# Kernel optimization log

Hardware: AMD Instinct MI355X
Metric: run time of the kernel (lower is better)

Reference implementation:

```python
import jax, jax.numpy as jnp
import numpy as np

N_BINS = 10


def setup_inputs() -> dict:
    key = jax.random.key(0)
    k1, k2 = jax.random.split(key)
    N, C = 1000000, 128
    logits = jax.random.normal(k1, (N, C), dtype=jnp.float32)
    labels = jax.random.randint(k2, (N,), 0, C, dtype=jnp.int64)
    return {"logits": logits, "labels": labels}


def reference(logits, labels):
    N = logits.shape[0]
    probs = jax.nn.softmax(logits, axis=1)
    confidences = jnp.max(probs, axis=1)          # [N]
    predictions = jnp.argmax(probs, axis=1)       # [N]
    accuracies = (predictions == labels).astype(jnp.float32)

    # Bin i covers (i/n, (i+1)/n]; ceil(conf*n)-1 gives that index.
    bin_idx = jnp.clip(
        jnp.ceil(confidences * N_BINS).astype(jnp.int32) - 1, 0, N_BINS - 1
    )

    counts = jax.ops.segment_sum(jnp.ones_like(confidences), bin_idx, num_segments=N_BINS)
    conf_sum = jax.ops.segment_sum(confidences, bin_idx, num_segments=N_BINS)
    acc_sum = jax.ops.segment_sum(accuracies, bin_idx, num_segments=N_BINS)

    prop_in_bin = counts / N
    nonempty = counts > 0
    denom = jnp.maximum(counts, 1.0)
    acc_in_bin = jnp.where(nonempty, acc_sum / denom, 0.0)
    conf_in_bin = jnp.where(nonempty, conf_sum / denom, 0.0)

    CE = conf_in_bin - acc_in_bin
    abs_CE = jnp.where(nonempty, jnp.abs(CE), 0.0)
    ece = jnp.sum(abs_CE * prop_in_bin)
    oe = jnp.sum(jnp.where(nonempty, conf_in_bin * jnp.maximum(CE, 0.0), 0.0) * prop_in_bin)

    # (ece, per-bin accuracy, oe, per-bin proportion, per-bin |CE|)
    return ece, acc_in_bin, oe, prop_in_bin, abs_CE
```

## Files before the change

### kernel.cpp

```cpp
#include <hip/hip_runtime.h>

#define N_BINS 10

template<int CTRL, bool BC>
__device__ __forceinline__ float dpp_f(float x, float old_) {
    int r = __builtin_amdgcn_update_dpp(__builtin_bit_cast(int, old_),
                                        __builtin_bit_cast(int, x),
                                        CTRL, 0xf, 0xf, BC);
    return __builtin_bit_cast(float, r);
}

__device__ __forceinline__ float half_reduce_add(float x) {
    x += dpp_f<0x111, true>(x, 0.f);
    x += dpp_f<0x112, true>(x, 0.f);
    x += dpp_f<0x114, true>(x, 0.f);
    x += dpp_f<0x118, true>(x, 0.f);
    x += dpp_f<0x142, true>(x, 0.f);
    return x;
}

__device__ __forceinline__ float half_reduce_max(float x) {
    x = fmaxf(x, dpp_f<0x111, false>(x, x));
    x = fmaxf(x, dpp_f<0x112, false>(x, x));
    x = fmaxf(x, dpp_f<0x114, false>(x, x));
    x = fmaxf(x, dpp_f<0x118, false>(x, x));
    x = fmaxf(x, dpp_f<0x142, false>(x, x));
    return x;
}

__global__ void ece_zero_ws(unsigned int* ws) {
    int i = threadIdx.x;
    if (i < 64) ws[i] = 0u;
}

__global__ __launch_bounds__(256) void ece_main(
        const float* __restrict__ logits,
        const int*   __restrict__ labels,
        float*       __restrict__ ws,
        int N) {
    __shared__ float              s_conf[N_BINS];
    __shared__ unsigned long long s_pack[N_BINS];
    if (threadIdx.x < N_BINS) {
        s_conf[threadIdx.x] = 0.f;
        s_pack[threadIdx.x] = 0ull;
    }
    __syncthreads();

    const int lane32       = threadIdx.x & 31;
    const int rowInBlock   = threadIdx.x >> 5;
    const int rowsPerBlock = blockDim.x >> 5;

    long long row = (long long)blockIdx.x * rowsPerBlock + rowInBlock;
    const long long rowStride = (long long)gridDim.x * rowsPerBlock;

    for (; row < N; row += rowStride) {
        const float4* p = (const float4*)(logits + row * 128);
        float4 v = p[lane32];
        int la = labels[row];

        float m4 = fmaxf(fmaxf(v.x, v.y), fmaxf(v.z, v.w));
        float e4 = __expf(v.x) + __expf(v.y) + __expf(v.z) + __expf(v.w);
        float vl = 0.f;
        if ((la >> 2) == lane32) {
            int r = la & 3;
            vl = (r == 0) ? v.x : (r == 1) ? v.y : (r == 2) ? v.z : v.w;
        }

        float S  = half_reduce_add(e4);
        float M  = half_reduce_max(m4);
        float VL = half_reduce_add(vl);

        if (lane32 == 31) {
            float conf = __expf(M) / S;
            int bin = (int)ceilf(conf * 10.0f) - 1;
            bin = min(max(bin, 0), N_BINS - 1);
            unsigned long long packed = 0x100000000ull | (unsigned long long)(VL == M ? 1u : 0u);
            atomicAdd(&s_conf[bin], conf);
            atomicAdd(&s_pack[bin], packed);
        }
    }

    __syncthreads();
    if (threadIdx.x < N_BINS) {
        atomicAdd(&ws[threadIdx.x], s_conf[threadIdx.x]);
        atomicAdd((unsigned long long*)((char*)ws + 64) + threadIdx.x, s_pack[threadIdx.x]);
    }
}

__global__ void ece_finalize(const float* __restrict__ ws, float* __restrict__ out, int N) {
    if (threadIdx.x == 0 && blockIdx.x == 0) {
        const unsigned long long* pack = (const unsigned long long*)((const char*)ws + 64);
        float ece = 0.f, oe = 0.f;
        for (int b = 0; b < N_BINS; ++b) {
            float cs = ws[b];
            unsigned long long pk = pack[b];
            unsigned int c  = (unsigned int)(pk >> 32);
            float as        = (float)(unsigned int)(pk & 0xffffffffull);
            float cnt   = (float)c;
            float prop  = cnt / (float)N;
            float denom = fmaxf(cnt, 1.0f);
            bool  ne    = (c > 0);
            float acc_in  = ne ? as / denom : 0.f;
            float conf_in = ne ? cs / denom : 0.f;
            float CE    = conf_in - acc_in;
            float absCE = ne ? fabsf(CE) : 0.f;
            ece += absCE * prop;
            oe  += (ne ? conf_in * fmaxf(CE, 0.f) : 0.f) * prop;
            out[1 + b]  = acc_in;
            out[12 + b] = prop;
            out[22 + b] = absCE;
        }
        out[0]  = ece;
        out[11] = oe;
    }
}

extern "C" void kernel_launch(void* const* d_in, const int* in_sizes, int n_in,
                              void* d_out, int out_size, void* d_ws, size_t ws_size,
                              hipStream_t stream) {
    const float* logits = (const float*)d_in[0];
    const int*   labels = (const int*)d_in[1];
    float*       out    = (float*)d_out;
    float*       ws     = (float*)d_ws;
    const int N = in_sizes[1];

    hipLaunchKernelGGL(ece_zero_ws, dim3(1), dim3(64), 0, stream, (unsigned int*)ws);

    const int block = 256;
    const int rowsPerBlock = block / 32;
    int grid = (N + rowsPerBlock - 1) / rowsPerBlock;
    if (grid > 2048) grid = 2048;
    hipLaunchKernelGGL(ece_main, dim3(grid), dim3(block), 0, stream,
                       logits, labels, ws, N);

    hipLaunchKernelGGL(ece_finalize, dim3(1), dim3(64), 0, stream, ws, out, N);
}
```

Baseline: 657.7 us.

## Process rows with 8 lanes each and software-prefetch next tile

Restructures the main loop so each group of 8 lanes handles one row, with each lane loading four float4s, and each wave covering 8 rows per tile. The next tile's loads are issued before the current tile is computed, a software-pipelined double buffer meant to hide memory latency. Reductions shrink from 5 DPP steps to 3. In exchange, register use per thread goes up, which may lower occupancy.

```diff
diff --git a/kernel.cpp b/kernel.cpp
--- a/kernel.cpp
+++ b/kernel.cpp
@@ -10,22 +10,43 @@
     return __builtin_bit_cast(float, r);
 }
 
-__device__ __forceinline__ float half_reduce_add(float x) {
+__device__ __forceinline__ float grp8_add(float x) {
     x += dpp_f<0x111, true>(x, 0.f);
     x += dpp_f<0x112, true>(x, 0.f);
     x += dpp_f<0x114, true>(x, 0.f);
-    x += dpp_f<0x118, true>(x, 0.f);
-    x += dpp_f<0x142, true>(x, 0.f);
+    return x;
+}
+__device__ __forceinline__ float grp8_max(float x) {
+    x = fmaxf(x, dpp_f<0x111, false>(x, x));
+    x = fmaxf(x, dpp_f<0x112, false>(x, x));
+    x = fmaxf(x, dpp_f<0x114, false>(x, x));
     return x;
 }
 
-__device__ __forceinline__ float half_reduce_max(float x) {
-    x = fmaxf(x, dpp_f<0x111, false>(x, x));
-    x = fmaxf(x, dpp_f<0x112, false>(x, x));
-    x = fmaxf(x, dpp_f<0x114, false>(x, x));
-    x = fmaxf(x, dpp_f<0x118, false>(x, x));
-    x = fmaxf(x, dpp_f<0x142, false>(x, x));
-    return x;
+struct Tile {
+    float4 v0, v1, v2, v3;
+    int    la;
+    bool   valid;
+};
+
+__device__ __forceinline__ Tile load_tile(const float* __restrict__ logits,
+                                          const int*   __restrict__ labels,
+                                          long long tile, int grp, int sub, int N) {
+    Tile d;
+    long long row = tile * 8 + grp;
+    d.valid = row < (long long)N;
+    if (d.valid) {
+        const float* rp = logits + row * 128 + sub * 4;
+        d.v0 = *(const float4*)(rp);
+        d.v1 = *(const float4*)(rp + 32);
+        d.v2 = *(const float4*)(rp + 64);
+        d.v3 = *(const float4*)(rp + 96);
+        d.la = labels[row];
+    } else {
+        d.v0 = d.v1 = d.v2 = d.v3 = make_float4(0.f, 0.f, 0.f, 0.f);
+        d.la = 0;
+    }
+    return d;
 }
 
 __global__ void ece_zero_ws(unsigned int* ws) {
@@ -46,31 +67,52 @@
     }
     __syncthreads();
 
-    const int lane32       = threadIdx.x & 31;
-    const int rowInBlock   = threadIdx.x >> 5;
-    const int rowsPerBlock = blockDim.x >> 5;
+    const int lane = threadIdx.x & 63;
+    const int sub  = lane & 7;
+    const int grp  = lane >> 3;
+    const int wid  = threadIdx.x >> 6;
 
-    long long row = (long long)blockIdx.x * rowsPerBlock + rowInBlock;
-    const long long rowStride = (long long)gridDim.x * rowsPerBlock;
+    long long tile = (long long)blockIdx.x * 4 + wid;
+    const long long tStride = (long long)gridDim.x * 4;
+    const long long nTiles  = ((long long)N + 7) >> 3;
 
-    for (; row < N; row += rowStride) {
-        const float4* p = (const float4*)(logits + row * 128);
-        float4 v = p[lane32];
-        int la = labels[row];
+    Tile cur = load_tile(logits, labels, tile, grp, sub, N);
 
-        float m4 = fmaxf(fmaxf(v.x, v.y), fmaxf(v.z, v.w));
-        float e4 = __expf(v.x) + __expf(v.y) + __expf(v.z) + __expf(v.w);
-        float vl = 0.f;
-        if ((la >> 2) == lane32) {
-            int r = la & 3;
-            vl = (r == 0) ? v.x : (r == 1) ? v.y : (r == 2) ? v.z : v.w;
+    while (tile < nTiles) {
+        long long ntile = tile + tStride;
+        Tile nxt;
+        if (ntile < nTiles) {
+            nxt = load_tile(logits, labels, ntile, grp, sub, N);
+        } else {
+            nxt.v0 = nxt.v1 = nxt.v2 = nxt.v3 = make_float4(0.f, 0.f, 0.f, 0.f);
+            nxt.la = 0; nxt.valid = false;
         }
 
-        float S  = half_reduce_add(e4);
-        float M  = half_reduce_max(m4);
-        float VL = half_reduce_add(vl);
+        float m0 = fmaxf(fmaxf(cur.v0.x, cur.v0.y), fmaxf(cur.v0.z, cur.v0.w));
+        float m1 = fmaxf(fmaxf(cur.v1.x, cur.v1.y), fmaxf(cur.v1.z, cur.v1.w));
+        float m2 = fmaxf(fmaxf(cur.v2.x, cur.v2.y), fmaxf(cur.v2.z, cur.v2.w));
+        float m3 = fmaxf(fmaxf(cur.v3.x, cur.v3.y), fmaxf(cur.v3.z, cur.v3.w));
+        float mL = fmaxf(fmaxf(m0, m1), fmaxf(m2, m3));
 
-        if (lane32 == 31) {
+        float e0 = __expf(cur.v0.x) + __expf(cur.v0.y) + __expf(cur.v0.z) + __expf(cur.v0.w);
+        float e1 = __expf(cur.v1.x) + __expf(cur.v1.y) + __expf(cur.v1.z) + __expf(cur.v1.w);
+        float e2 = __expf(cur.v2.x) + __expf(cur.v2.y) + __expf(cur.v2.z) + __expf(cur.v2.w);
+        float e3 = __expf(cur.v3.x) + __expf(cur.v3.y) + __expf(cur.v3.z) + __expf(cur.v3.w);
+        float e  = (e0 + e1) + (e2 + e3);
+
+        float vl = 0.f;
+        if ((((unsigned)cur.la >> 2) & 7u) == (unsigned)sub) {
+            int lj = cur.la >> 5;
+            int lr = cur.la & 3;
+            float4 vv = (lj == 0) ? cur.v0 : (lj == 1) ? cur.v1 : (lj == 2) ? cur.v2 : cur.v3;
+            vl = (lr == 0) ? vv.x : (lr == 1) ? vv.y : (lr == 2) ? vv.z : vv.w;
+        }
+
+        float S  = grp8_add(e);
+        float M  = grp8_max(mL);
+        float VL = grp8_add(vl);
+
+        if (sub == 7 && cur.valid) {
             float conf = __expf(M) / S;
             int bin = (int)ceilf(conf * 10.0f) - 1;
             bin = min(max(bin, 0), N_BINS - 1);
@@ -78,6 +120,9 @@
             atomicAdd(&s_conf[bin], conf);
             atomicAdd(&s_pack[bin], packed);
         }
+
+        cur  = nxt;
+        tile = ntile;
     }
 
     __syncthreads();
@@ -127,9 +172,9 @@
     hipLaunchKernelGGL(ece_zero_ws, dim3(1), dim3(64), 0, stream, (unsigned int*)ws);
 
     const int block = 256;
-    const int rowsPerBlock = block / 32;
-    int grid = (N + rowsPerBlock - 1) / rowsPerBlock;
-    if (grid > 2048) grid = 2048;
+    long long nTiles = ((long long)N + 7) >> 3;
+    long long g = (nTiles + 3) / 4;
+    int grid = (g > 2048) ? 2048 : (int)g;
     hipLaunchKernelGGL(ece_main, dim3(grid), dim3(block), 0, stream,
                        logits, labels, ws, N);
 
```

Result: slower. 690.5 us (+5.0%).
